# Performance work log

Measured on AMD Instinct MI355X. Metric: run time of the kernel, lower is better.

## Reference

```python
import jax, jax.numpy as jnp
import numpy as np

T, STATE_DIM, ACTION_DIM = 1024, 1024, 64
D, S, H = 2048, 1024, 2048  # deterministic, stochastic, hidden (= embedding_size)


def _lin_init(k, out_dim, in_dim):
    k1, k2 = jax.random.split(k)
    lim = 1.0 / np.sqrt(in_dim)
    w = jax.random.uniform(k1, (out_dim, in_dim), minval=-lim, maxval=lim, dtype=jnp.float32)
    b = jax.random.uniform(k2, (out_dim,), minval=-lim, maxval=lim, dtype=jnp.float32)
    return w, b


def setup_inputs() -> dict:
    key = jax.random.key(0)
    ks = jax.random.split(key, 16)
    enc_w, enc_b = _lin_init(ks[0], H, STATE_DIM)                 # WorldModel.encoder
    dec_w, dec_b = _lin_init(ks[1], STATE_DIM + 2, S + D)         # WorldModel.decoder
    p_enc_w, p_enc_b = _lin_init(ks[2], D, S + ACTION_DIM)        # Prior.encoder
    glim = 1.0 / np.sqrt(D)
    gru_wih = jax.random.uniform(ks[3], (3 * D, D), minval=-glim, maxval=glim, dtype=jnp.float32)
    gru_whh = jax.random.uniform(ks[4], (3 * D, D), minval=-glim, maxval=glim, dtype=jnp.float32)
    gru_b = jax.random.uniform(ks[5], (3 * D,), minval=-glim, maxval=glim, dtype=jnp.float32)
    gru_bn = jax.random.uniform(ks[6], (D,), minval=-glim, maxval=glim, dtype=jnp.float32)
    p_dec1_w, p_dec1_b = _lin_init(ks[7], H, D)                   # Prior.decoder1
    p_dec2_w, p_dec2_b = _lin_init(ks[8], 2 * S, H)               # Prior.decoder2
    q_enc_w, q_enc_b = _lin_init(ks[9], H, D + H)                 # Posterior.encoder
    q_dec_w, q_dec_b = _lin_init(ks[10], 2 * S, H)                # Posterior.decoder
    observation = jax.random.normal(ks[11], (T, STATE_DIM), dtype=jnp.float32)
    actions = jax.random.normal(ks[12], (T, ACTION_DIM), dtype=jnp.float32)
    noise = jax.random.normal(ks[13], (T, S), dtype=jnp.float32)  # reparam eps for posterior sample
    return dict(observation=observation, actions=actions, noise=noise,
                enc_w=enc_w, enc_b=enc_b, dec_w=dec_w, dec_b=dec_b,
                p_enc_w=p_enc_w, p_enc_b=p_enc_b,
                gru_wih=gru_wih, gru_whh=gru_whh, gru_b=gru_b, gru_bn=gru_bn,
                p_dec1_w=p_dec1_w, p_dec1_b=p_dec1_b, p_dec2_w=p_dec2_w, p_dec2_b=p_dec2_b,
                q_enc_w=q_enc_w, q_enc_b=q_enc_b, q_dec_w=q_dec_w, q_dec_b=q_dec_b)


def reference(observation, actions, noise, enc_w, enc_b, dec_w, dec_b,
              p_enc_w, p_enc_b, gru_wih, gru_whh, gru_b, gru_bn,
              p_dec1_w, p_dec1_b, p_dec2_w, p_dec2_b,
              q_enc_w, q_enc_b, q_dec_w, q_dec_b):
    elu = jax.nn.elu
    # obs embeddings: [T, H]
    emb = elu(observation @ enc_w.T + enc_b)

    def step(carry, inp):
        stoch_prev, det_prev = carry
        e, act, eps = inp
        # Prior: encoder -> GRU -> decoder1 -> decoder2
        x = elu(p_enc_w @ jnp.concatenate([stoch_prev, act]) + p_enc_b)  # [D]
        ig = gru_wih @ x + gru_b
        hg = gru_whh @ det_prev
        ir, iz, inw = jnp.split(ig, 3)
        hr, hz, hn = jnp.split(hg, 3)
        r = jax.nn.sigmoid(ir + hr)
        z = jax.nn.sigmoid(iz + hz)
        n = jnp.tanh(inw + r * (hn + gru_bn))
        det = n + z * (det_prev - n)                                     # GRU hidden [D]
        y = elu(p_dec1_w @ det + p_dec1_b)
        y = p_dec2_w @ y + p_dec2_b
        pmu, pstd = jnp.split(y, 2)
        pstd = jax.nn.softplus(pstd) + 0.1
        # Posterior on (det, embedding)
        q = elu(q_enc_w @ jnp.concatenate([det, e]) + q_enc_b)
        q = q_dec_w @ q + q_dec_b
        qmu, qstd = jnp.split(q, 2)
        qstd = jax.nn.softplus(qstd) + 0.1
        stoch = qmu + qstd * eps                                         # Normal sample (reparam)
        return (stoch, det), (stoch, det, qmu, qstd, pmu, pstd)

    init = (jnp.zeros(S, observation.dtype), jnp.zeros(D, observation.dtype))
    _, (stoch, det, qmu, qstd, pmu, pstd) = jax.lax.scan(step, init, (emb, actions, noise))
    states_flat = jnp.concatenate([stoch, det], axis=-1)                  # [T, S+D]
    outs = states_flat @ dec_w.T + dec_b                                  # [T, state_dim+2]
    return stoch, det, outs, qmu, qstd, pmu, pstd


if __name__ == '__main__':
    out = reference(**setup_inputs())
    for o in out:
        print(o.shape)
```

## Files before the change

kernel.cpp:

```cpp
#include <hip/hip_runtime.h>
#include <cstdint>
#include <cstddef>

#define T_STEPS 1024
#define S_DIM   1024
#define A_DIM   64
#define D_DIM   2048
#define H_DIM   2048
#define NWG     256
#define NTHR    512

typedef unsigned short ushort_t;
typedef unsigned long long u64;

__device__ __forceinline__ float eluf(float v)      { return v > 0.f ? v : expm1f(v); }
__device__ __forceinline__ float softplusf(float v) { return v > 20.f ? v : log1pf(expf(v)); }
__device__ __forceinline__ float sigmoidf_(float v) { return 1.f / (1.f + expf(-v)); }

__device__ __forceinline__ float wave_reduce(float v) {
  #pragma unroll
  for (int off = 32; off > 0; off >>= 1) v += __shfl_xor(v, off, 64);
  return v;
}

__device__ __forceinline__ float2 bf2(unsigned u) {
  float2 r;
  r.x = __uint_as_float(u << 16);
  r.y = __uint_as_float(u & 0xffff0000u);
  return r;
}
__device__ __forceinline__ ushort_t f2bf_rne(float f) {
  unsigned u = __float_as_uint(f);
  u += 0x7fffu + ((u >> 16) & 1u);
  return (ushort_t)(u >> 16);
}

#define LD_PIN_U4(dst, addr) \
  asm volatile("global_load_dwordx4 %0, %1, off" : "=v"(dst) : "v"(addr))

__device__ __forceinline__ void st_rec(u64* p, float v, unsigned g) {
  const u64 r = (u64)__float_as_uint(v) | ((u64)g << 32);
  __hip_atomic_store(p, r, __ATOMIC_RELAXED, __HIP_MEMORY_SCOPE_AGENT);
}
__device__ __forceinline__ u64 ld_rec(const u64* p) {
  return __hip_atomic_load(p, __ATOMIC_RELAXED, __HIP_MEMORY_SCOPE_AGENT);
}

__device__ __forceinline__ void poll_pair(const u64* __restrict__ q0,
                                          const u64* __restrict__ q1,
                                          unsigned g, uint4& a, uint4& b) {
  int spins = 0;
  for (;;) {
    asm volatile("global_load_dwordx4 %0, %2, off sc1\n\t"
                 "global_load_dwordx4 %1, %3, off sc1\n\t"
                 "s_waitcnt vmcnt(0)"
                 : "=v"(a), "=v"(b) : "v"(q0), "v"(q1) : "memory");
    if (__all(a.y == g && a.w == g && b.y == g && b.w == g)) return;
    if (++spins > 4096) {
      const u64 c0 = ld_rec(q0), c1 = ld_rec(q0 + 1);
      const u64 c2 = ld_rec(q1), c3 = ld_rec(q1 + 1);
      a.x = (unsigned)c0; a.y = (unsigned)(c0 >> 32);
      a.z = (unsigned)c1; a.w = (unsigned)(c1 >> 32);
      b.x = (unsigned)c2; b.y = (unsigned)(c2 >> 32);
      b.z = (unsigned)c3; b.w = (unsigned)(c3 >> 32);
      if (__all(a.y == g && a.w == g && b.y == g && b.w == g)) return;
    }
    __builtin_amdgcn_s_sleep(1);
  }
}

__device__ __forceinline__ void poll4c(const u64* __restrict__ base, int i4,
                                       unsigned g, float* __restrict__ lds) {
  uint4 a, b;
  poll_pair(base + i4, base + i4 + 2, g, a, b);
  float4 out;
  out.x = __uint_as_float(a.x);
  out.y = __uint_as_float(a.z);
  out.z = __uint_as_float(b.x);
  out.w = __uint_as_float(b.z);
  *(float4*)(lds + i4) = out;
}

__global__ void init_recs(u64* r) {
  #pragma unroll
  for (int i = 0; i < 32; ++i) r[i * 256 + threadIdx.x] = 0ull;
}

__global__ __launch_bounds__(256) void pack_lin(
    const float* __restrict__ src, unsigned* __restrict__ dst,
    int src_ld, int lc, size_t total_u32)
{
  for (size_t u = (size_t)blockIdx.x * 256 + threadIdx.x; u < total_u32;
       u += (size_t)gridDim.x * 256) {
    const size_t pos = u * 2;
    const size_t row = pos >> lc;
    const int    col = (int)(pos & (((size_t)1 << lc) - 1));
    const float2 v = *(const float2*)(src + row * src_ld + col);
    dst[u] = (unsigned)f2bf_rne(v.x) | ((unsigned)f2bf_rne(v.y) << 16);
  }
}

__global__ __launch_bounds__(256) void pack_swz(
    const float* __restrict__ src, unsigned* __restrict__ dst,
    int src_ld, int lc, size_t total2)
{
  for (size_t u = (size_t)blockIdx.x * 256 + threadIdx.x; u < total2;
       u += (size_t)gridDim.x * 256) {
    const size_t pos = u * 2;
    const size_t row = pos >> lc;
    const int pcol  = (int)(pos & (((size_t)1 << lc) - 1));
    const int chunk = pcol >> 9;
    const int off   = pcol & 511;
    const int l     = off >> 3;
    const int p     = (off >> 1) & 3;
    const float2 v  = *(const float2*)(src + row * src_ld + chunk * 512 + p * 128 + l * 2);
    dst[u] = (unsigned)f2bf_rne(v.x) | ((unsigned)f2bf_rne(v.y) << 16);
  }
}

__device__ __forceinline__ float chunk_dot(const uint4 w, const float* vchunk, int lane) {
  float acc = 0.f; float2 p, a;
  a = *(const float2*)(vchunk + lane * 2 +   0); p = bf2(w.x); acc += p.x*a.x + p.y*a.y;
  a = *(const float2*)(vchunk + lane * 2 + 128); p = bf2(w.y); acc += p.x*a.x + p.y*a.y;
  a = *(const float2*)(vchunk + lane * 2 + 256); p = bf2(w.z); acc += p.x*a.x + p.y*a.y;
  a = *(const float2*)(vchunk + lane * 2 + 384); p = bf2(w.w); acc += p.x*a.x + p.y*a.y;
  return acc;
}

__global__ __launch_bounds__(NTHR) void rssm_seq(
    const float* __restrict__ pre_act, const float* __restrict__ pre_e,
    u64* __restrict__ rec_mu, u64* __restrict__ rec_sd,
    u64* __restrict__ rec_x,  u64* __restrict__ rec_d, u64* __restrict__ rec_q,
    const unsigned* __restrict__ wps_lin,
    const unsigned* __restrict__ wih_lin,
    const ushort_t* __restrict__ whh_swz,
    const ushort_t* __restrict__ wqe_swz,
    const ushort_t* __restrict__ wqd_swz,
    const float* __restrict__ gru_b, const float* __restrict__ gru_bn,
    const float* __restrict__ q_dec_b, const float* __restrict__ noise,
    float* __restrict__ stoch_out, float* __restrict__ det_out,
    float* __restrict__ qmu_out, float* __restrict__ qstd_out)
{
  __shared__ float    xs[2048];
  __shared__ float    ds[2048];
  __shared__ float    qs[2048];
  __shared__ float    sp[1024];
  __shared__ unsigned wps_l[8 * 512];
  __shared__ unsigned wih_l[24 * 1024];

  const int tid  = threadIdx.x;
  const int wv   = tid >> 6;
  const int lane = tid & 63;
  const int bid  = blockIdx.x;
  const int r0   = bid * 8;

  #pragma unroll
  for (int i = 0; i < 8; ++i) {
    const int idx = i * NTHR + tid;
    const int row = idx >> 9, u = idx & 511;
    wps_l[idx] = wps_lin[((size_t)(r0 + row) << 9) | u];
  }
  #pragma unroll
  for (int i = 0; i < 48; ++i) {
    const int idx = i * NTHR + tid;
    const int gr = idx >> 10, u = idx & 1023;
    const int g = gr >> 3, rr = gr & 7;
    wih_l[idx] = wih_lin[((size_t)(g * 2048 + r0 + rr) << 10) | u];
  }

  uint4 w2h[12];
  uint4 w3[4];
  uint4 w4[4];
  {
    const size_t i = (size_t)(r0 + wv);
    #pragma unroll
    for (int g = 0; g < 3; ++g) {
      const uint4* wr = (const uint4*)(whh_swz + (i + (size_t)g * 2048) * 2048);
      #pragma unroll
      for (int c = 0; c < 4; ++c) LD_PIN_U4(w2h[g * 4 + c], wr + c * 64 + lane);
    }
    const uint4* we = (const uint4*)(wqe_swz + i * 2048);
    #pragma unroll
    for (int c = 0; c < 4; ++c) LD_PIN_U4(w3[c], we + c * 64 + lane);
    const int jg = bid * 4 + (wv & 3), sel = wv >> 2;
    const uint4* wd = (const uint4*)(wqd_swz + (size_t)(jg + sel * 1024) * 2048);
    #pragma unroll
    for (int c = 0; c < 4; ++c) LD_PIN_U4(w4[c], wd + c * 64 + lane);
    asm volatile("s_waitcnt vmcnt(0)" ::: "memory");
  }

  float gb_r = 0.f, gb_z = 0.f, gb_n = 0.f, gbn = 0.f, qdb = 0.f;
  if (lane == 0) {
    gb_r = gru_b[r0 + wv];
    gb_z = gru_b[r0 + wv + 2048];
    gb_n = gru_b[r0 + wv + 4096];
    gbn  = gru_bn[r0 + wv];
    qdb  = (wv < 4) ? q_dec_b[bid * 4 + wv] : q_dec_b[bid * 4 + (wv - 4) + 1024];
  }

  if (tid < 256) ((float4*)sp)[tid] = float4{0.f, 0.f, 0.f, 0.f};
  ((float4*)ds)[tid] = float4{0.f, 0.f, 0.f, 0.f};
  __syncthreads();

  for (int t = 0; t < T_STEPS; ++t) {
    const unsigned gb = (unsigned)(t * 4);
    float pa = 0.f, pe = 0.f;
    if (lane == 0) {
      pa = pre_act[(size_t)t * D_DIM + r0 + wv];
      pe = pre_e  [(size_t)t * H_DIM + r0 + wv];
    }

    if (t > 0) {
      const float2 e = *(const float2*)(noise + (size_t)(t - 1) * S_DIM + 2 * tid);
      uint4 m, s;
      poll_pair(rec_mu + 2 * tid, rec_sd + 2 * tid, gb, m, s);
      float2 sv;
      sv.x = __uint_as_float(m.x) + __uint_as_float(s.x) * e.x;
      sv.y = __uint_as_float(m.z) + __uint_as_float(s.z) * e.y;
      *(float2*)(sp + 2 * tid) = sv;
      if (bid == 0)
        *(float2*)(stoch_out + (size_t)(t - 1) * S_DIM + 2 * tid) = sv;
    }
    __syncthreads();
    {
      const unsigned* wrow = wps_l + (wv << 9);
      float acc = 0.f;
      #pragma unroll
      for (int c = 0; c < 2; ++c)
        #pragma unroll
        for (int p = 0; p < 4; ++p) {
          const float2 a = *(const float2*)(sp + c * 512 + p * 128 + lane * 2);
          const float2 w = bf2(wrow[c * 256 + p * 64 + lane]);
          acc += w.x * a.x + w.y * a.y;
        }
      acc = wave_reduce(acc);
      if (lane == 0) st_rec(rec_x + r0 + wv, eluf(acc + pa), gb + 1);
    }

    float h0 = 0.f, h1 = 0.f, h2 = 0.f;
    #pragma unroll
    for (int c = 0; c < 4; ++c) {
      #pragma unroll
      for (int p = 0; p < 4; ++p) {
        const float2 dv = *(const float2*)(ds + c * 512 + p * 128 + lane * 2);
        const unsigned u0 = (p == 0) ? w2h[c].x     : (p == 1) ? w2h[c].y     : (p == 2) ? w2h[c].z     : w2h[c].w;
        const unsigned u1 = (p == 0) ? w2h[4 + c].x : (p == 1) ? w2h[4 + c].y : (p == 2) ? w2h[4 + c].z : w2h[4 + c].w;
        const unsigned u2 = (p == 0) ? w2h[8 + c].x : (p == 1) ? w2h[8 + c].y : (p == 2) ? w2h[8 + c].z : w2h[8 + c].w;
        float2 w;
        w = bf2(u0); h0 += w.x * dv.x + w.y * dv.y;
        w = bf2(u1); h1 += w.x * dv.x + w.y * dv.y;
        w = bf2(u2); h2 += w.x * dv.x + w.y * dv.y;
      }
    }
    h0 = wave_reduce(h0); h1 = wave_reduce(h1); h2 = wave_reduce(h2);
    poll4c(rec_x, 4 * tid, gb + 1, xs);
    __syncthreads();
    {
      const unsigned* wg0 = wih_l + wv * 1024;
      const unsigned* wg1 = wg0 + 8192;
      const unsigned* wg2 = wg1 + 8192;
      float a0 = 0.f, a1 = 0.f, a2 = 0.f;
      #pragma unroll
      for (int c = 0; c < 4; ++c) {
        #pragma unroll
        for (int p = 0; p < 4; ++p) {
          const float2 xv = *(const float2*)(xs + c * 512 + p * 128 + lane * 2);
          const int wi = c * 256 + p * 64 + lane;
          float2 w;
          w = bf2(wg0[wi]); a0 += w.x * xv.x + w.y * xv.y;
          w = bf2(wg1[wi]); a1 += w.x * xv.x + w.y * xv.y;
          w = bf2(wg2[wi]); a2 += w.x * xv.x + w.y * xv.y;
        }
      }
      a0 = wave_reduce(a0); a1 = wave_reduce(a1); a2 = wave_reduce(a2);
      if (lane == 0) {
        const float r_ = sigmoidf_(a0 + gb_r + h0);
        const float z_ = sigmoidf_(a1 + gb_z + h1);
        const float n_ = tanhf(a2 + gb_n + r_ * (h2 + gbn));
        const float dv_ = n_ + z_ * (ds[r0 + wv] - n_);
        st_rec(rec_d + r0 + wv, dv_, gb + 2);
        det_out[(size_t)t * D_DIM + r0 + wv] = dv_;
      }
    }
    __syncthreads();

    poll4c(rec_d, 4 * tid, gb + 2, ds);
    __syncthreads();
    {
      float acc = 0.f;
      #pragma unroll
      for (int c = 0; c < 4; ++c) acc += chunk_dot(w3[c], ds + c * 512, lane);
      acc = wave_reduce(acc);
      if (lane == 0) st_rec(rec_q + r0 + wv, eluf(acc + pe), gb + 3);
    }

    poll4c(rec_q, 4 * tid, gb + 3, qs);
    __syncthreads();
    {
      float acc = 0.f;
      #pragma unroll
      for (int c = 0; c < 4; ++c) acc += chunk_dot(w4[c], qs + c * 512, lane);
      acc = wave_reduce(acc);
      if (lane == 0) {
        const int j = bid * 4 + (wv & 3);
        if (wv < 4) {
          const float qm = acc + qdb;
          st_rec(rec_mu + j, qm, gb + 4);
          qmu_out[(size_t)t * S_DIM + j] = qm;
        } else {
          const float qsd = softplusf(acc + qdb) + 0.1f;
          st_rec(rec_sd + j, qsd, gb + 4);
          qstd_out[(size_t)t * S_DIM + j] = qsd;
        }
      }
    }
  }

  if (bid == 0) {
    const unsigned gf = (unsigned)(T_STEPS * 4);
    const float2 e = *(const float2*)(noise + (size_t)(T_STEPS - 1) * S_DIM + 2 * tid);
    uint4 m, s;
    poll_pair(rec_mu + 2 * tid, rec_sd + 2 * tid, gf, m, s);
    float2 sv;
    sv.x = __uint_as_float(m.x) + __uint_as_float(s.x) * e.x;
    sv.y = __uint_as_float(m.z) + __uint_as_float(s.z) * e.y;
    *(float2*)(stoch_out + (size_t)(T_STEPS - 1) * S_DIM + 2 * tid) = sv;
  }
}

template <int ACT>
__global__ __launch_bounds__(256) void gemm_xwT(
    const float* __restrict__ X1, int ldx1,
    const float* __restrict__ X2, int ldx2, int ksplit,
    const float* __restrict__ W, int ldw, int woff,
    const float* __restrict__ bias,
    float* __restrict__ C, int ldc,
    int M, int N, int K)
{
  __shared__ float Xs[16][65];
  __shared__ float Ws[16][65];
  const int tid = threadIdx.x;
  const int tx = tid & 15, ty = tid >> 4;
  const int m0 = blockIdx.y * 64, n0 = blockIdx.x * 64;
  const int lrow = tid >> 2;
  const int kq4  = (tid & 3) * 4;
  float acc[4][4] = {};
  for (int k0 = 0; k0 < K; k0 += 16) {
    {
      const int m = m0 + lrow;
      #pragma unroll
      for (int j = 0; j < 4; ++j) {
        const int k = k0 + kq4 + j;
        float v = 0.f;
        if (m < M)
          v = (k < ksplit) ? X1[(size_t)m * ldx1 + k]
                           : X2[(size_t)m * ldx2 + (k - ksplit)];
        Xs[kq4 + j][lrow] = v;
      }
      const int n = n0 + lrow;
      #pragma unroll
      for (int j = 0; j < 4; ++j) {
        const int k = k0 + kq4 + j;
        Ws[kq4 + j][lrow] = (n < N) ? W[(size_t)n * ldw + woff + k] : 0.f;
      }
    }
    __syncthreads();
    #pragma unroll
    for (int kk = 0; kk < 16; ++kk) {
      float a[4], b[4];
      #pragma unroll
      for (int i = 0; i < 4; ++i) a[i] = Xs[kk][ty * 4 + i];
      #pragma unroll
      for (int j = 0; j < 4; ++j) b[j] = Ws[kk][tx * 4 + j];
      #pragma unroll
      for (int i = 0; i < 4; ++i)
        #pragma unroll
        for (int j = 0; j < 4; ++j)
          acc[i][j] += a[i] * b[j];
    }
    __syncthreads();
  }
  #pragma unroll
  for (int i = 0; i < 4; ++i) {
    const int m = m0 + ty * 4 + i;
    if (m >= M) continue;
    #pragma unroll
    for (int j = 0; j < 4; ++j) {
      const int n = n0 + tx * 4 + j;
      if (n >= N) continue;
      float v = acc[i][j] + bias[n];
      if (ACT == 1) v = eluf(v);
      if (ACT == 2) {
        if (n < 1024) C[(size_t)m * 1024 + n] = v;
        else          C[(size_t)m * 1024 + (n - 1024) + 1024 * 1024] = softplusf(v) + 0.1f;
      } else {
        C[(size_t)m * ldc + n] = v;
      }
    }
  }
}

extern "C" void kernel_launch(void* const* d_in, const int* in_sizes, int n_in,
                              void* d_out, int out_size, void* d_ws, size_t ws_size,
                              hipStream_t stream)
{
  const float* obs      = (const float*)d_in[0];
  const float* acts     = (const float*)d_in[1];
  const float* noise    = (const float*)d_in[2];
  const float* enc_w    = (const float*)d_in[3];
  const float* enc_b    = (const float*)d_in[4];
  const float* dec_w    = (const float*)d_in[5];
  const float* dec_b    = (const float*)d_in[6];
  const float* p_enc_w  = (const float*)d_in[7];
  const float* p_enc_b  = (const float*)d_in[8];
  const float* gru_wih  = (const float*)d_in[9];
  const float* gru_whh  = (const float*)d_in[10];
  const float* gru_b    = (const float*)d_in[11];
  const float* gru_bn   = (const float*)d_in[12];
  const float* p_dec1_w = (const float*)d_in[13];
  const float* p_dec1_b = (const float*)d_in[14];
  const float* p_dec2_w = (const float*)d_in[15];
  const float* p_dec2_b = (const float*)d_in[16];
  const float* q_enc_w  = (const float*)d_in[17];
  const float* q_enc_b  = (const float*)d_in[18];
  const float* q_dec_w  = (const float*)d_in[19];
  const float* q_dec_b  = (const float*)d_in[20];

  float* out   = (float*)d_out;
  float* stoch = out;
  float* det   = out + 1048576;
  float* outs  = out + 3145728;
  float* qmu   = out + 4196352;
  float* qstd  = out + 5244928;
  float* pmu   = out + 6293504;

  u64* rec_mu = (u64*)outs;
  u64* rec_sd = rec_mu + 1024;
  u64* rec_x  = rec_sd + 1024;
  u64* rec_d  = rec_x + 2048;
  u64* rec_q  = rec_d + 2048;

  float* ws       = (float*)d_ws;
  float* pre_act  = ws;
  float* pre_e    = ws + 2097152;
  float* emb      = ws + 4194304;
  ushort_t* wpack = (ushort_t*)(ws + 6299648);
  ushort_t* wps_lin = wpack;
  ushort_t* wih_lin = wps_lin + 2097152;
  ushort_t* whh_swz = wih_lin + 12582912;
  ushort_t* wqe_swz = whh_swz + 12582912;
  ushort_t* wqd_swz = wqe_swz + 4194304;

  init_recs<<<dim3(1), dim3(256), 0, stream>>>(rec_mu);

  pack_lin<<<dim3(1024), dim3(256), 0, stream>>>(p_enc_w, (unsigned*)wps_lin, 1088, 10, 1048576);
  pack_lin<<<dim3(1024), dim3(256), 0, stream>>>(gru_wih, (unsigned*)wih_lin, 2048, 11, 6291456);
  pack_swz<<<dim3(1024), dim3(256), 0, stream>>>(gru_whh, (unsigned*)whh_swz, 2048, 11, 6291456);
  pack_swz<<<dim3(1024), dim3(256), 0, stream>>>(q_enc_w, (unsigned*)wqe_swz, 4096, 11, 2097152);
  pack_swz<<<dim3(1024), dim3(256), 0, stream>>>(q_dec_w, (unsigned*)wqd_swz, 2048, 11, 2097152);

  dim3 blk(256);
  gemm_xwT<0><<<dim3(32, 16), blk, 0, stream>>>(
      acts, 64, acts, 64, 64, p_enc_w, 1088, 1024, p_enc_b, pre_act, 2048, 1024, 2048, 64);
  gemm_xwT<1><<<dim3(32, 16), blk, 0, stream>>>(
      obs, 1024, obs, 1024, 1024, enc_w, 1024, 0, enc_b, emb, 2048, 1024, 2048, 1024);
  gemm_xwT<0><<<dim3(32, 16), blk, 0, stream>>>(
      emb, 2048, emb, 2048, 2048, q_enc_w, 4096, 2048, q_enc_b, pre_e, 2048, 1024, 2048, 2048);

  rssm_seq<<<dim3(NWG), dim3(NTHR), 0, stream>>>(
      pre_act, pre_e, rec_mu, rec_sd, rec_x, rec_d, rec_q,
      (const unsigned*)wps_lin, (const unsigned*)wih_lin,
      whh_swz, wqe_swz, wqd_swz,
      gru_b, gru_bn, q_dec_b, noise, stoch, det, qmu, qstd);

  gemm_xwT<1><<<dim3(32, 16), blk, 0, stream>>>(
      det, 2048, det, 2048, 2048, p_dec1_w, 2048, 0, p_dec1_b, emb, 2048, 1024, 2048, 2048);
  gemm_xwT<2><<<dim3(32, 16), blk, 0, stream>>>(
      emb, 2048, emb, 2048, 2048, p_dec2_w, 2048, 0, p_dec2_b, pmu, 1024, 1024, 2048, 2048);
  gemm_xwT<0><<<dim3(17, 16), blk, 0, stream>>>(
      stoch, 1024, det, 2048, 1024, dec_w, 3072, 0, dec_b, outs, 1026, 1024, 1026, 3072);
}
```

Baseline: 20.32 ms.

## Replace per-element tagged records with sharded arrival counters for grid sync

Drops the scheme where every published value carried a generation tag in a 64-bit record and consumers polled all records. Producers now write plain floats, then one thread per block bumps one of 16 sharded atomic counters. Consumers spin on those 16 counters until they reach the target and then bulk-load the values. This halves the bytes moved per exchange and shrinks polling to 16 words, but adds a block-wide barrier, a waitcnt and an atomic per phase, and relies on relaxed ordering between the data stores and the counter increment.

```diff
diff --git a/kernel.cpp b/kernel.cpp
--- a/kernel.cpp
+++ b/kernel.cpp
@@ -11,7 +11,6 @@
 #define NTHR    512
 
 typedef unsigned short ushort_t;
-typedef unsigned long long u64;
 
 __device__ __forceinline__ float eluf(float v)      { return v > 0.f ? v : expm1f(v); }
 __device__ __forceinline__ float softplusf(float v) { return v > 20.f ? v : log1pf(expf(v)); }
@@ -38,52 +37,36 @@
 #define LD_PIN_U4(dst, addr) \
   asm volatile("global_load_dwordx4 %0, %1, off" : "=v"(dst) : "v"(addr))
 
-__device__ __forceinline__ void st_rec(u64* p, float v, unsigned g) {
-  const u64 r = (u64)__float_as_uint(v) | ((u64)g << 32);
-  __hip_atomic_store(p, r, __ATOMIC_RELAXED, __HIP_MEMORY_SCOPE_AGENT);
-}
-__device__ __forceinline__ u64 ld_rec(const u64* p) {
-  return __hip_atomic_load(p, __ATOMIC_RELAXED, __HIP_MEMORY_SCOPE_AGENT);
-}
-
-__device__ __forceinline__ void poll_pair(const u64* __restrict__ q0,
-                                          const u64* __restrict__ q1,
-                                          unsigned g, uint4& a, uint4& b) {
-  int spins = 0;
+__device__ __forceinline__ void st_val(float* p, float v) {
+  __hip_atomic_store((unsigned*)p, __float_as_uint(v),
+                     __ATOMIC_RELAXED, __HIP_MEMORY_SCOPE_AGENT);
+}
+
+__device__ __forceinline__ void wait_cnt(const unsigned* cbase, unsigned target, int lane) {
+  const unsigned* p = cbase + (lane & 15);
   for (;;) {
-    asm volatile("global_load_dwordx4 %0, %2, off sc1\n\t"
-                 "global_load_dwordx4 %1, %3, off sc1\n\t"
-                 "s_waitcnt vmcnt(0)"
-                 : "=v"(a), "=v"(b) : "v"(q0), "v"(q1) : "memory");
-    if (__all(a.y == g && a.w == g && b.y == g && b.w == g)) return;
-    if (++spins > 4096) {
-      const u64 c0 = ld_rec(q0), c1 = ld_rec(q0 + 1);
-      const u64 c2 = ld_rec(q1), c3 = ld_rec(q1 + 1);
-      a.x = (unsigned)c0; a.y = (unsigned)(c0 >> 32);
-      a.z = (unsigned)c1; a.w = (unsigned)(c1 >> 32);
-      b.x = (unsigned)c2; b.y = (unsigned)(c2 >> 32);
-      b.z = (unsigned)c3; b.w = (unsigned)(c3 >> 32);
-      if (__all(a.y == g && a.w == g && b.y == g && b.w == g)) return;
-    }
+    unsigned c;
+    asm volatile("global_load_dword %0, %1, off sc1\n\ts_waitcnt vmcnt(0)"
+                 : "=v"(c) : "v"(p) : "memory");
+    if (__all(c >= target)) return;
     __builtin_amdgcn_s_sleep(1);
   }
 }
 
-__device__ __forceinline__ void poll4c(const u64* __restrict__ base, int i4,
-                                       unsigned g, float* __restrict__ lds) {
-  uint4 a, b;
-  poll_pair(base + i4, base + i4 + 2, g, a, b);
-  float4 out;
-  out.x = __uint_as_float(a.x);
-  out.y = __uint_as_float(a.z);
-  out.z = __uint_as_float(b.x);
-  out.w = __uint_as_float(b.z);
-  *(float4*)(lds + i4) = out;
-}
-
-__global__ void init_recs(u64* r) {
+__device__ __forceinline__ void bulk4(const float* __restrict__ src, int i4,
+                                      float* __restrict__ lds) {
+  float4 v;
+  asm volatile("global_load_dwordx4 %0, %1, off sc1\n\ts_waitcnt vmcnt(0)"
+               : "=v"(v) : "v"(src + i4) : "memory");
+  *(float4*)(lds + i4) = v;
+}
+
+__global__ void init_sync(unsigned* c) {
   #pragma unroll
-  for (int i = 0; i < 32; ++i) r[i * 256 + threadIdx.x] = 0ull;
+  for (int i = 0; i < 33; ++i) {
+    const int idx = i * 256 + threadIdx.x;
+    if (idx < 8256) c[idx] = 0u;
+  }
 }
 
 __global__ __launch_bounds__(256) void pack_lin(
@@ -129,8 +112,9 @@
 
 __global__ __launch_bounds__(NTHR) void rssm_seq(
     const float* __restrict__ pre_act, const float* __restrict__ pre_e,
-    u64* __restrict__ rec_mu, u64* __restrict__ rec_sd,
-    u64* __restrict__ rec_x,  u64* __restrict__ rec_d, u64* __restrict__ rec_q,
+    unsigned* __restrict__ cnt,
+    float* __restrict__ muv, float* __restrict__ sdv,
+    float* __restrict__ xv,  float* __restrict__ dv, float* __restrict__ qv,
     const unsigned* __restrict__ wps_lin,
     const unsigned* __restrict__ wih_lin,
     const ushort_t* __restrict__ whh_swz,
@@ -153,6 +137,7 @@
   const int lane = tid & 63;
   const int bid  = blockIdx.x;
   const int r0   = bid * 8;
+  const int cslot = bid & 15;
 
   #pragma unroll
   for (int i = 0; i < 8; ++i) {
@@ -203,7 +188,7 @@
   __syncthreads();
 
   for (int t = 0; t < T_STEPS; ++t) {
-    const unsigned gb = (unsigned)(t * 4);
+    const unsigned tgt = 16u * (unsigned)(t + 1);
     float pa = 0.f, pe = 0.f;
     if (lane == 0) {
       pa = pre_act[(size_t)t * D_DIM + r0 + wv];
@@ -211,12 +196,16 @@
     }
 
     if (t > 0) {
+      wait_cnt(cnt + 48, 16u * (unsigned)t, lane);
       const float2 e = *(const float2*)(noise + (size_t)(t - 1) * S_DIM + 2 * tid);
-      uint4 m, s;
-      poll_pair(rec_mu + 2 * tid, rec_sd + 2 * tid, gb, m, s);
+      float2 m, s;
+      asm volatile("global_load_dwordx2 %0, %2, off sc1\n\t"
+                   "global_load_dwordx2 %1, %3, off sc1\n\t"
+                   "s_waitcnt vmcnt(0)"
+                   : "=v"(m), "=v"(s) : "v"(muv + 2 * tid), "v"(sdv + 2 * tid) : "memory");
       float2 sv;
-      sv.x = __uint_as_float(m.x) + __uint_as_float(s.x) * e.x;
-      sv.y = __uint_as_float(m.z) + __uint_as_float(s.z) * e.y;
+      sv.x = m.x + s.x * e.x;
+      sv.y = m.y + s.y * e.y;
       *(float2*)(sp + 2 * tid) = sv;
       if (bid == 0)
         *(float2*)(stoch_out + (size_t)(t - 1) * S_DIM + 2 * tid) = sv;
@@ -234,26 +223,31 @@
           acc += w.x * a.x + w.y * a.y;
         }
       acc = wave_reduce(acc);
-      if (lane == 0) st_rec(rec_x + r0 + wv, eluf(acc + pa), gb + 1);
-    }
+      if (lane == 0) st_val(xv + r0 + wv, eluf(acc + pa));
+      asm volatile("s_waitcnt vmcnt(0)" ::: "memory");
+    }
+    __syncthreads();
+    if (tid == 0)
+      __hip_atomic_fetch_add(cnt + cslot, 1u, __ATOMIC_RELAXED, __HIP_MEMORY_SCOPE_AGENT);
 
     float h0 = 0.f, h1 = 0.f, h2 = 0.f;
     #pragma unroll
     for (int c = 0; c < 4; ++c) {
       #pragma unroll
       for (int p = 0; p < 4; ++p) {
-        const float2 dv = *(const float2*)(ds + c * 512 + p * 128 + lane * 2);
+        const float2 dvv = *(const float2*)(ds + c * 512 + p * 128 + lane * 2);
         const unsigned u0 = (p == 0) ? w2h[c].x     : (p == 1) ? w2h[c].y     : (p == 2) ? w2h[c].z     : w2h[c].w;
         const unsigned u1 = (p == 0) ? w2h[4 + c].x : (p == 1) ? w2h[4 + c].y : (p == 2) ? w2h[4 + c].z : w2h[4 + c].w;
         const unsigned u2 = (p == 0) ? w2h[8 + c].x : (p == 1) ? w2h[8 + c].y : (p == 2) ? w2h[8 + c].z : w2h[8 + c].w;
         float2 w;
-        w = bf2(u0); h0 += w.x * dv.x + w.y * dv.y;
-        w = bf2(u1); h1 += w.x * dv.x + w.y * dv.y;
-        w = bf2(u2); h2 += w.x * dv.x + w.y * dv.y;
+        w = bf2(u0); h0 += w.x * dvv.x + w.y * dvv.y;
+        w = bf2(u1); h1 += w.x * dvv.x + w.y * dvv.y;
+        w = bf2(u2); h2 += w.x * dvv.x + w.y * dvv.y;
       }
     }
     h0 = wave_reduce(h0); h1 = wave_reduce(h1); h2 = wave_reduce(h2);
-    poll4c(rec_x, 4 * tid, gb + 1, xs);
+    wait_cnt(cnt, tgt, lane);
+    bulk4(xv, 4 * tid, xs);
     __syncthreads();
     {
       const unsigned* wg0 = wih_l + wv * 1024;
@@ -264,12 +258,12 @@
       for (int c = 0; c < 4; ++c) {
         #pragma unroll
         for (int p = 0; p < 4; ++p) {
-          const float2 xv = *(const float2*)(xs + c * 512 + p * 128 + lane * 2);
+          const float2 xvv = *(const float2*)(xs + c * 512 + p * 128 + lane * 2);
           const int wi = c * 256 + p * 64 + lane;
           float2 w;
-          w = bf2(wg0[wi]); a0 += w.x * xv.x + w.y * xv.y;
-          w = bf2(wg1[wi]); a1 += w.x * xv.x + w.y * xv.y;
-          w = bf2(wg2[wi]); a2 += w.x * xv.x + w.y * xv.y;
+          w = bf2(wg0[wi]); a0 += w.x * xvv.x + w.y * xvv.y;
+          w = bf2(wg1[wi]); a1 += w.x * xvv.x + w.y * xvv.y;
+          w = bf2(wg2[wi]); a2 += w.x * xvv.x + w.y * xvv.y;
         }
       }
       a0 = wave_reduce(a0); a1 = wave_reduce(a1); a2 = wave_reduce(a2);
@@ -277,24 +271,33 @@
         const float r_ = sigmoidf_(a0 + gb_r + h0);
         const float z_ = sigmoidf_(a1 + gb_z + h1);
         const float n_ = tanhf(a2 + gb_n + r_ * (h2 + gbn));
-        const float dv_ = n_ + z_ * (ds[r0 + wv] - n_);
-        st_rec(rec_d + r0 + wv, dv_, gb + 2);
-        det_out[(size_t)t * D_DIM + r0 + wv] = dv_;
-      }
-    }
-    __syncthreads();
-
-    poll4c(rec_d, 4 * tid, gb + 2, ds);
+        const float det_v = n_ + z_ * (ds[r0 + wv] - n_);
+        st_val(dv + r0 + wv, det_v);
+        det_out[(size_t)t * D_DIM + r0 + wv] = det_v;
+      }
+      asm volatile("s_waitcnt vmcnt(0)" ::: "memory");
+    }
+    __syncthreads();
+    if (tid == 0)
+      __hip_atomic_fetch_add(cnt + 16 + cslot, 1u, __ATOMIC_RELAXED, __HIP_MEMORY_SCOPE_AGENT);
+
+    wait_cnt(cnt + 16, tgt, lane);
+    bulk4(dv, 4 * tid, ds);
     __syncthreads();
     {
       float acc = 0.f;
       #pragma unroll
       for (int c = 0; c < 4; ++c) acc += chunk_dot(w3[c], ds + c * 512, lane);
       acc = wave_reduce(acc);
-      if (lane == 0) st_rec(rec_q + r0 + wv, eluf(acc + pe), gb + 3);
-    }
-
-    poll4c(rec_q, 4 * tid, gb + 3, qs);
+      if (lane == 0) st_val(qv + r0 + wv, eluf(acc + pe));
+      asm volatile("s_waitcnt vmcnt(0)" ::: "memory");
+    }
+    __syncthreads();
+    if (tid == 0)
+      __hip_atomic_fetch_add(cnt + 32 + cslot, 1u, __ATOMIC_RELAXED, __HIP_MEMORY_SCOPE_AGENT);
+
+    wait_cnt(cnt + 32, tgt, lane);
+    bulk4(qv, 4 * tid, qs);
     __syncthreads();
     {
       float acc = 0.f;
@@ -305,25 +308,32 @@
         const int j = bid * 4 + (wv & 3);
         if (wv < 4) {
           const float qm = acc + qdb;
-          st_rec(rec_mu + j, qm, gb + 4);
+          st_val(muv + j, qm);
           qmu_out[(size_t)t * S_DIM + j] = qm;
         } else {
           const float qsd = softplusf(acc + qdb) + 0.1f;
-          st_rec(rec_sd + j, qsd, gb + 4);
+          st_val(sdv + j, qsd);
           qstd_out[(size_t)t * S_DIM + j] = qsd;
         }
       }
-    }
+      asm volatile("s_waitcnt vmcnt(0)" ::: "memory");
+    }
+    __syncthreads();
+    if (tid == 0)
+      __hip_atomic_fetch_add(cnt + 48 + cslot, 1u, __ATOMIC_RELAXED, __HIP_MEMORY_SCOPE_AGENT);
   }
 
   if (bid == 0) {
-    const unsigned gf = (unsigned)(T_STEPS * 4);
+    wait_cnt(cnt + 48, 16u * (unsigned)T_STEPS, lane);
     const float2 e = *(const float2*)(noise + (size_t)(T_STEPS - 1) * S_DIM + 2 * tid);
-    uint4 m, s;
-    poll_pair(rec_mu + 2 * tid, rec_sd + 2 * tid, gf, m, s);
+    float2 m, s;
+    asm volatile("global_load_dwordx2 %0, %2, off sc1\n\t"
+                 "global_load_dwordx2 %1, %3, off sc1\n\t"
+                 "s_waitcnt vmcnt(0)"
+                 : "=v"(m), "=v"(s) : "v"(muv + 2 * tid), "v"(sdv + 2 * tid) : "memory");
     float2 sv;
-    sv.x = __uint_as_float(m.x) + __uint_as_float(s.x) * e.x;
-    sv.y = __uint_as_float(m.z) + __uint_as_float(s.z) * e.y;
+    sv.x = m.x + s.x * e.x;
+    sv.y = m.y + s.y * e.y;
     *(float2*)(stoch_out + (size_t)(T_STEPS - 1) * S_DIM + 2 * tid) = sv;
   }
 }
@@ -434,11 +444,12 @@
   float* qstd  = out + 5244928;
   float* pmu   = out + 6293504;
 
-  u64* rec_mu = (u64*)outs;
-  u64* rec_sd = rec_mu + 1024;
-  u64* rec_x  = rec_sd + 1024;
-  u64* rec_d  = rec_x + 2048;
-  u64* rec_q  = rec_d + 2048;
+  unsigned* cnt = (unsigned*)outs;
+  float* muv = outs + 64;
+  float* sdv = muv + 1024;
+  float* xv  = sdv + 1024;
+  float* dvv = xv + 2048;
+  float* qvv = dvv + 2048;
 
   float* ws       = (float*)d_ws;
   float* pre_act  = ws;
@@ -451,7 +462,7 @@
   ushort_t* wqe_swz = whh_swz + 12582912;
   ushort_t* wqd_swz = wqe_swz + 4194304;
 
-  init_recs<<<dim3(1), dim3(256), 0, stream>>>(rec_mu);
+  init_sync<<<dim3(1), dim3(256), 0, stream>>>(cnt);
 
   pack_lin<<<dim3(1024), dim3(256), 0, stream>>>(p_enc_w, (unsigned*)wps_lin, 1088, 10, 1048576);
   pack_lin<<<dim3(1024), dim3(256), 0, stream>>>(gru_wih, (unsigned*)wih_lin, 2048, 11, 6291456);
@@ -468,7 +479,7 @@
       emb, 2048, emb, 2048, 2048, q_enc_w, 4096, 2048, q_enc_b, pre_e, 2048, 1024, 2048, 2048);
 
   rssm_seq<<<dim3(NWG), dim3(NTHR), 0, stream>>>(
-      pre_act, pre_e, rec_mu, rec_sd, rec_x, rec_d, rec_q,
+      pre_act, pre_e, cnt, muv, sdv, xv, dvv, qvv,
       (const unsigned*)wps_lin, (const unsigned*)wih_lin,
       whh_swz, wqe_swz, wqd_swz,
       gru_b, gru_bn, q_dec_b, noise, stoch, det, qmu, qstd);
```

After: 57.49 ms. 2.83x slower.
